# Optimization experiments

Measured on AMD Instinct MI355X. Metric: run time of the kernel, lower is better.

Reference implementation:

```python
import jax, jax.numpy as jnp
import numpy as np

B, T = 8192, 2048
DT = 1.0


def setup_inputs() -> dict:
    key = jax.random.key(0)
    k1, k2, k3 = jax.random.split(key, 3)
    price = jax.random.normal(k1, (B, T), dtype=jnp.float32)
    hurst = jax.random.uniform(k2, (B, T), dtype=jnp.float32)
    vol_sigma = jax.random.uniform(k3, (B, T), dtype=jnp.float32)
    return {"price": price, "hurst": hurst, "vol_sigma": vol_sigma}


def _ekf(price, hurst, vol_sigma):
    dt = DT
    b = price.shape[0]
    dtype = price.dtype
    eye2 = jnp.eye(2, dtype=dtype)
    # initial state: [price_0, (price_1 - price_0)/dt]
    v0 = (price[:, 1] - price[:, 0]) / dt
    x0 = jnp.stack([price[:, 0], v0], axis=1)               # [B,2]
    P0 = jnp.broadcast_to(eye2, (b, 2, 2))                  # [B,2,2]

    e1 = jnp.array([1.0, 0.0], dtype=dtype)                 # H row = [1,0]

    def step(carry, inp):
        x, P = carry                                        # [B,2], [B,2,2]
        z, h, sig = inp                                     # each [B]
        rho = 0.5 + 0.5 * jax.nn.sigmoid(10.0 * (h - 0.5))
        a = dt * rho                                        # F[:,0,1]
        ones = jnp.ones_like(a)
        zeros = jnp.zeros_like(a)
        # F = [[1, a],[0, 1]] per batch element
        F = jnp.stack([jnp.stack([ones, a], -1),
                       jnp.stack([zeros, ones], -1)], axis=1)  # [B,2,2]
        scale = jnp.maximum(100.0 * sig, 1.0)               # clamp(min=1)
        # predict
        x_pred = jnp.einsum('bij,bj->bi', F, x)
        P_pred = jnp.einsum('bij,bjk,blk->bil', F, P, F) \
                 + (0.1 * scale)[:, None, None] * eye2      # + Q
        # update (H = [1,0] observes position only)
        y = z - x_pred[:, 0]                                # residual [B]
        S = P_pred[:, 0, 0] + scale                         # + R
        S_inv = 1.0 / (S + 1e-6)
        K = P_pred[:, :, 0] * S_inv[:, None]                # [B,2]
        x_new = x_pred + K * y[:, None]
        ImKH = eye2 - K[:, :, None] * e1[None, None, :]     # I - K H
        P_new = jnp.einsum('bij,bjk->bik', ImKH, P_pred)
        return (x_new, P_new), x_new

    xs = (price.T, hurst.T, vol_sigma.T)                    # [T,B] each
    _, states = jax.lax.scan(step, (x0, P0), xs)            # states: [T,B,2]
    return jnp.transpose(states, (1, 0, 2))                 # [B,T,2]


def reference(price, hurst, vol_sigma):
    return _ekf(price, hurst, vol_sigma)
```

## Files before the change

kernel.cpp:

```cpp
#include <hip/hip_runtime.h>


#define NB 8192
#define NT 2048
#define TPB 128
#define SEG 16
#define NC4 4
#define LSTRIDE 130

__device__ __forceinline__ float frcp(float x)  { return __builtin_amdgcn_rcpf(x); }
__device__ __forceinline__ float fexp2(float x) { return __builtin_amdgcn_exp2f(x); }

struct Elt {
    float A00, A01, A10, A11;
    float b0, b1;
    float C00, C01, C11;
    float e0, e1;
    float J00, J01, J11;
};

__device__ __forceinline__ Elt combine(const Elt& i, const Elt& j)
{
    float D00 = 1.0f + __builtin_fmaf(i.C00, j.J00, i.C01 * j.J01);
    float D01 =        __builtin_fmaf(i.C00, j.J01, i.C01 * j.J11);
    float D10 =        __builtin_fmaf(i.C01, j.J00, i.C11 * j.J01);
    float D11 = 1.0f + __builtin_fmaf(i.C01, j.J01, i.C11 * j.J11);
    float idet = frcp(__builtin_fmaf(D00, D11, -D01 * D10));
    float V00 =  D11 * idet, V01 = -D01 * idet;
    float V10 = -D10 * idet, V11 =  D00 * idet;
    float E00 = __builtin_fmaf(j.A00, V00, j.A01 * V10);
    float E01 = __builtin_fmaf(j.A00, V01, j.A01 * V11);
    float E10 = __builtin_fmaf(j.A10, V00, j.A11 * V10);
    float E11 = __builtin_fmaf(j.A10, V01, j.A11 * V11);
    Elt r;
    r.A00 = __builtin_fmaf(E00, i.A00, E01 * i.A10);
    r.A01 = __builtin_fmaf(E00, i.A01, E01 * i.A11);
    r.A10 = __builtin_fmaf(E10, i.A00, E11 * i.A10);
    r.A11 = __builtin_fmaf(E10, i.A01, E11 * i.A11);
    float t0 = i.b0 + __builtin_fmaf(i.C00, j.e0, i.C01 * j.e1);
    float t1 = i.b1 + __builtin_fmaf(i.C01, j.e0, i.C11 * j.e1);
    r.b0 = j.b0 + __builtin_fmaf(E00, t0, E01 * t1);
    r.b1 = j.b1 + __builtin_fmaf(E10, t0, E11 * t1);
    float T00 = __builtin_fmaf(E00, i.C00, E01 * i.C01);
    float T01 = __builtin_fmaf(E00, i.C01, E01 * i.C11);
    float T10 = __builtin_fmaf(E10, i.C00, E11 * i.C01);
    float T11 = __builtin_fmaf(E10, i.C01, E11 * i.C11);
    r.C00 = j.C00 + __builtin_fmaf(T00, j.A00, T01 * j.A01);
    r.C01 = j.C01 + __builtin_fmaf(T00, j.A10, T01 * j.A11);
    r.C11 = j.C11 + __builtin_fmaf(T10, j.A10, T11 * j.A11);
    float u0 = j.e0 - __builtin_fmaf(j.J00, i.b0, j.J01 * i.b1);
    float u1 = j.e1 - __builtin_fmaf(j.J01, i.b0, j.J11 * i.b1);
    float w0 = __builtin_fmaf(V00, u0, V10 * u1);
    float w1 = __builtin_fmaf(V01, u0, V11 * u1);
    r.e0 = i.e0 + __builtin_fmaf(i.A00, w0, i.A10 * w1);
    r.e1 = i.e1 + __builtin_fmaf(i.A01, w0, i.A11 * w1);
    float W00 = __builtin_fmaf(V00, j.J00, V10 * j.J01);
    float W01 = __builtin_fmaf(V00, j.J01, V10 * j.J11);
    float W10 = __builtin_fmaf(V01, j.J00, V11 * j.J01);
    float W11 = __builtin_fmaf(V01, j.J01, V11 * j.J11);
    float X00 = __builtin_fmaf(i.A00, W00, i.A10 * W10);
    float X01 = __builtin_fmaf(i.A00, W01, i.A10 * W11);
    float X10 = __builtin_fmaf(i.A01, W00, i.A11 * W10);
    float X11 = __builtin_fmaf(i.A01, W01, i.A11 * W11);
    r.J00 = i.J00 + __builtin_fmaf(X00, i.A00, X01 * i.A10);
    r.J01 = i.J01 + __builtin_fmaf(X00, i.A01, X01 * i.A11);
    r.J11 = i.J11 + __builtin_fmaf(X10, i.A01, X11 * i.A11);
    return r;
}

__device__ __forceinline__ void append_step(Elt& E, float z, float h, float sg,
                                            float& a_out, float& sc_out)
{
    float ee = fexp2(__builtin_fmaf(h, -14.4269504088896f, 7.2134752044448f));
    float a  = __builtin_fmaf(0.5f, frcp(1.0f + ee), 0.5f);
    float sc = fmaxf(100.0f * sg, 1.0f);
    float q  = 0.1f * sc;
    float r  = sc + 1e-6f;
    float Sinv = frcp(q + r);
    float u = q * Sinv;
    float v = r * Sinv;
    a_out = a; sc_out = sc;

    float cw0 = __builtin_fmaf(a, E.C01, E.C00);
    float cw1 = __builtin_fmaf(a, E.C11, E.C01);
    float g0 = Sinv * cw0, g1 = Sinv * cw1;
    float rho = frcp(__builtin_fmaf(a, g1, 1.0f + g0));
    float gp0 = rho * g0, gp1 = rho * g1;

    float s0 = __builtin_fmaf(a, E.A10, E.A00);
    float s1 = __builtin_fmaf(a, E.A11, E.A01);

    float wb0  = __builtin_fmaf(a, E.b1, E.b0);
    float beta = Sinv * (z - wb0);
    float bp0  = __builtin_fmaf(z, g0, E.b0);
    float bp1  = __builtin_fmaf(z, g1, E.b1);

    float N00 = __builtin_fmaf(-gp0, s0, E.A00);
    float N01 = __builtin_fmaf(-gp0, s1, E.A01);
    float N10 = __builtin_fmaf(-gp1, s0, E.A10);
    float N11 = __builtin_fmaf(-gp1, s1, E.A11);
    float A00n = v * __builtin_fmaf(a, N10, N00);
    float A01n = v * __builtin_fmaf(a, N11, N01);
    float wbp = __builtin_fmaf(a, bp1, bp0);
    float t0b = __builtin_fmaf(-gp0, wbp, bp0);
    float t1b = __builtin_fmaf(-gp1, wbp, bp1);
    float b0n = __builtin_fmaf(v, __builtin_fmaf(a, t1b, t0b), u * z);
    float M00 = __builtin_fmaf(-gp0, cw0, E.C00);
    float M01 = __builtin_fmaf(-gp0, cw1, E.C01);
    float M11 = __builtin_fmaf(-gp1, cw1, E.C11);
    float tc0 = __builtin_fmaf(a, M01, M00);
    float tc1 = __builtin_fmaf(a, M11, M01);
    float C00n = v * __builtin_fmaf(v, __builtin_fmaf(a, tc1, tc0), q);
    float C01n = v * tc1;
    float C11n = M11 + q;
    float br  = beta * rho;
    float e0n = __builtin_fmaf(br, s0, E.e0);
    float e1n = __builtin_fmaf(br, s1, E.e1);
    float kap = rho * Sinv;
    float ks0 = kap * s0, ks1 = kap * s1;
    float J00n = __builtin_fmaf(ks0, s0, E.J00);
    float J01n = __builtin_fmaf(ks0, s1, E.J01);
    float J11n = __builtin_fmaf(ks1, s1, E.J11);

    E.A00 = A00n; E.A01 = A01n; E.A10 = N10; E.A11 = N11;
    E.b0 = b0n;  E.b1 = t1b;
    E.C00 = C00n; E.C01 = C01n; E.C11 = C11n;
    E.e0 = e0n;  E.e1 = e1n;
    E.J00 = J00n; E.J01 = J01n; E.J11 = J11n;
}

__device__ __forceinline__ Elt shfl_up_elt(const Elt& x, int d)
{
    Elt r;
    r.A00 = __shfl_up(x.A00, d, 64); r.A01 = __shfl_up(x.A01, d, 64);
    r.A10 = __shfl_up(x.A10, d, 64); r.A11 = __shfl_up(x.A11, d, 64);
    r.b0  = __shfl_up(x.b0,  d, 64); r.b1  = __shfl_up(x.b1,  d, 64);
    r.C00 = __shfl_up(x.C00, d, 64); r.C01 = __shfl_up(x.C01, d, 64);
    r.C11 = __shfl_up(x.C11, d, 64);
    r.e0  = __shfl_up(x.e0,  d, 64); r.e1  = __shfl_up(x.e1,  d, 64);
    r.J00 = __shfl_up(x.J00, d, 64); r.J01 = __shfl_up(x.J01, d, 64);
    r.J11 = __shfl_up(x.J11, d, 64);
    return r;
}

__device__ __forceinline__ void replay_step(float z, float a, float sc,
        float& x0, float& x1, float& p00, float& p01, float& p11)
{
    float q  = 0.1f * sc;
    float rp = sc + 1e-6f;
    float qr = q + rp;
    float tA = __builtin_fmaf(a + a, p01, p00);
    float tB = __builtin_fmaf(a * a, p11, qr);
    float Seff = tA + tB;
    float Sinv = frcp(Seff);
    float pp00 = Seff - rp;
    float pp01 = __builtin_fmaf(a, p11, p01);
    float pp11 = p11 + q;
    float K0 = pp00 * Sinv, K1 = pp01 * Sinv;
    float xp0 = __builtin_fmaf(a, x1, x0);
    float y = z - xp0;
    x0 = __builtin_fmaf(K0, y, xp0);
    x1 = __builtin_fmaf(K1, y, x1);
    p00 = __builtin_fmaf(-K0, pp00, pp00);
    p01 = __builtin_fmaf(-K0, pp01, pp01);
    p11 = __builtin_fmaf(-K1, pp01, pp11);
}

__global__ __launch_bounds__(TPB)
void ekf_kernel(const float* __restrict__ price,
                const float* __restrict__ hurst,
                const float* __restrict__ sigv,
                float* __restrict__ out)
{
    __shared__ float2 xlds[SEG][LSTRIDE];
    __shared__ float  w0tot[14];

    const int row  = blockIdx.x;
    const int tid  = threadIdx.x;
    const int lane = tid & 63;
    const int wav  = tid >> 6;

    const float4* __restrict__ pr4 = (const float4*)(price + (size_t)row * NT) + tid * NC4;
    const float4* __restrict__ hu4 = (const float4*)(hurst + (size_t)row * NT) + tid * NC4;
    const float4* __restrict__ sg4 = (const float4*)(sigv  + (size_t)row * NT) + tid * NC4;

    const float* __restrict__ prow = price + (size_t)row * NT;
    const float m00 = prow[0];
    const float m01 = prow[1] - m00;

    Elt E;
    E.A00 = 1.0f; E.A01 = 0.0f; E.A10 = 0.0f; E.A11 = 1.0f;
    E.b0 = 0.0f; E.b1 = 0.0f;
    E.C00 = 0.0f; E.C01 = 0.0f; E.C11 = 0.0f;
    E.e0 = 0.0f; E.e1 = 0.0f;
    E.J00 = 0.0f; E.J01 = 0.0f; E.J11 = 0.0f;
    {
        float4 zb[NC4], hb[NC4], sb[NC4];
#pragma unroll
        for (int c = 0; c < NC4; ++c) zb[c] = pr4[c];
#pragma unroll
        for (int c = 0; c < NC4; ++c) hb[c] = hu4[c];
#pragma unroll
        for (int c = 0; c < NC4; ++c) sb[c] = sg4[c];

#pragma unroll
        for (int c = 0; c < NC4; ++c) {
            float a0, c0, a1, c1, a2, c2, a3, c3;
            append_step(E, zb[c].x, hb[c].x, sb[c].x, a0, c0);
            append_step(E, zb[c].y, hb[c].y, sb[c].y, a1, c1);
            append_step(E, zb[c].z, hb[c].z, sb[c].z, a2, c2);
            append_step(E, zb[c].w, hb[c].w, sb[c].w, a3, c3);
            const int k = 4 * c;
            xlds[k + 0][tid] = make_float2(a0, c0);
            xlds[k + 1][tid] = make_float2(a1, c1);
            xlds[k + 2][tid] = make_float2(a2, c2);
            xlds[k + 3][tid] = make_float2(a3, c3);
        }
    }

#pragma unroll
    for (int d = 1; d < 64; d <<= 1) {
        Elt o = shfl_up_elt(E, d);
        Elt c = combine(o, E);
        bool p = (lane >= d);
        E.A00 = p ? c.A00 : E.A00; E.A01 = p ? c.A01 : E.A01;
        E.A10 = p ? c.A10 : E.A10; E.A11 = p ? c.A11 : E.A11;
        E.b0  = p ? c.b0  : E.b0;  E.b1  = p ? c.b1  : E.b1;
        E.C00 = p ? c.C00 : E.C00; E.C01 = p ? c.C01 : E.C01;
        E.C11 = p ? c.C11 : E.C11;
        E.e0  = p ? c.e0  : E.e0;  E.e1  = p ? c.e1  : E.e1;
        E.J00 = p ? c.J00 : E.J00; E.J01 = p ? c.J01 : E.J01;
        E.J11 = p ? c.J11 : E.J11;
    }

    if (tid == 63) {
        w0tot[0]  = E.A00; w0tot[1]  = E.A01; w0tot[2]  = E.A10; w0tot[3]  = E.A11;
        w0tot[4]  = E.b0;  w0tot[5]  = E.b1;
        w0tot[6]  = E.C00; w0tot[7]  = E.C01; w0tot[8]  = E.C11;
        w0tot[9]  = E.e0;  w0tot[10] = E.e1;
        w0tot[11] = E.J00; w0tot[12] = E.J01; w0tot[13] = E.J11;
    }
    __syncthreads();

    Elt ex = shfl_up_elt(E, 1);
    {
        bool l0 = (lane == 0);
        ex.A00 = l0 ? 1.0f : ex.A00; ex.A01 = l0 ? 0.0f : ex.A01;
        ex.A10 = l0 ? 0.0f : ex.A10; ex.A11 = l0 ? 1.0f : ex.A11;
        ex.b0  = l0 ? 0.0f : ex.b0;  ex.b1  = l0 ? 0.0f : ex.b1;
        ex.C00 = l0 ? 0.0f : ex.C00; ex.C01 = l0 ? 0.0f : ex.C01;
        ex.C11 = l0 ? 0.0f : ex.C11;
        ex.e0  = l0 ? 0.0f : ex.e0;  ex.e1  = l0 ? 0.0f : ex.e1;
        ex.J00 = l0 ? 0.0f : ex.J00; ex.J01 = l0 ? 0.0f : ex.J01;
        ex.J11 = l0 ? 0.0f : ex.J11;
    }
    if (wav == 1) {
        Elt w0;
        w0.A00 = w0tot[0];  w0.A01 = w0tot[1];  w0.A10 = w0tot[2];  w0.A11 = w0tot[3];
        w0.b0  = w0tot[4];  w0.b1  = w0tot[5];
        w0.C00 = w0tot[6];  w0.C01 = w0tot[7];  w0.C11 = w0tot[8];
        w0.e0  = w0tot[9];  w0.e1  = w0tot[10];
        w0.J00 = w0tot[11]; w0.J01 = w0tot[12]; w0.J11 = w0tot[13];
        ex = combine(w0, ex);
    }

    float D00 = 1.0f + ex.J00, D01 = ex.J01, D11 = 1.0f + ex.J11;
    float idet = frcp(__builtin_fmaf(D00, D11, -D01 * D01));
    float V00 =  D11 * idet, V01 = -D01 * idet;
    float V10 = -D01 * idet, V11 =  D00 * idet;
    float E00 = __builtin_fmaf(ex.A00, V00, ex.A01 * V10);
    float E01 = __builtin_fmaf(ex.A00, V01, ex.A01 * V11);
    float E10 = __builtin_fmaf(ex.A10, V00, ex.A11 * V10);
    float E11 = __builtin_fmaf(ex.A10, V01, ex.A11 * V11);
    float t0 = m00 + ex.e0, t1 = m01 + ex.e1;
    float x0 = ex.b0 + __builtin_fmaf(E00, t0, E01 * t1);
    float x1 = ex.b1 + __builtin_fmaf(E10, t0, E11 * t1);
    float p00 = ex.C00 + __builtin_fmaf(E00, ex.A00, E01 * ex.A01);
    float p01 = ex.C01 + __builtin_fmaf(E00, ex.A10, E01 * ex.A11);
    float p11 = ex.C11 + __builtin_fmaf(E10, ex.A10, E11 * ex.A11);

    {
        float4 zb[NC4];
#pragma unroll
        for (int c = 0; c < NC4; ++c) zb[c] = pr4[c];

#pragma unroll
        for (int c = 0; c < NC4; ++c) {
            const int k = 4 * c;
            float2 q0 = xlds[k + 0][tid];
            float2 q1 = xlds[k + 1][tid];
            float2 q2 = xlds[k + 2][tid];
            float2 q3 = xlds[k + 3][tid];

            replay_step(zb[c].x, q0.x, q0.y, x0, x1, p00, p01, p11);
            xlds[k + 0][tid] = make_float2(x0, x1);
            replay_step(zb[c].y, q1.x, q1.y, x0, x1, p00, p01, p11);
            xlds[k + 1][tid] = make_float2(x0, x1);
            replay_step(zb[c].z, q2.x, q2.y, x0, x1, p00, p01, p11);
            xlds[k + 2][tid] = make_float2(x0, x1);
            replay_step(zb[c].w, q3.x, q3.y, x0, x1, p00, p01, p11);
            xlds[k + 3][tid] = make_float2(x0, x1);
        }
    }
    __syncthreads();

    float2* __restrict__ op2 = (float2*)(out + (size_t)row * (size_t)NT * 2);
#pragma unroll
    for (int w = 0; w < SEG; ++w) {
        int n = w * TPB + tid;
        op2[n] = xlds[n & 15][n >> 4];
    }
}

extern "C" void kernel_launch(void* const* d_in, const int* in_sizes, int n_in,
                              void* d_out, int out_size, void* d_ws, size_t ws_size,
                              hipStream_t stream)
{
    const float* price = (const float*)d_in[0];
    const float* hurst = (const float*)d_in[1];
    const float* sigv  = (const float*)d_in[2];
    float* out = (float*)d_out;

    dim3 grid(NB), block(TPB);
    hipLaunchKernelGGL(ekf_kernel, grid, block, 0, stream, price, hurst, sigv, out);
}
```

Before: 278.0 us.

## Keep per-step coefficients in registers and write outputs directly from each thread

The per-step (a, scale) coefficients are now kept in a 16-entry register array instead of being staged in LDS. The LDS transpose buffer and its barrier are removed, and each thread stores its 16 contiguous float2 outputs straight to global memory. This cuts LDS traffic and a __syncthreads, but raises register pressure and makes the global stores strided across lanes (128 B apart) rather than fully coalesced.

Result: slower. 308.0 us (+10.8%).

```diff
diff --git a/kernel.cpp b/kernel.cpp
--- a/kernel.cpp
+++ b/kernel.cpp
@@ -6,7 +6,6 @@
 #define TPB 128
 #define SEG 16
 #define NC4 4
-#define LSTRIDE 130
 
 __device__ __forceinline__ float frcp(float x)  { return __builtin_amdgcn_rcpf(x); }
 __device__ __forceinline__ float fexp2(float x) { return __builtin_amdgcn_exp2f(x); }
@@ -68,18 +67,21 @@
     return r;
 }
 
-__device__ __forceinline__ void append_step(Elt& E, float z, float h, float sg,
-                                            float& a_out, float& sc_out)
+__device__ __forceinline__ float2 cvt_asc(float h, float sg)
 {
     float ee = fexp2(__builtin_fmaf(h, -14.4269504088896f, 7.2134752044448f));
     float a  = __builtin_fmaf(0.5f, frcp(1.0f + ee), 0.5f);
     float sc = fmaxf(100.0f * sg, 1.0f);
+    return make_float2(a, sc);
+}
+
+__device__ __forceinline__ void append_step(Elt& E, float z, float a, float sc)
+{
     float q  = 0.1f * sc;
     float r  = sc + 1e-6f;
     float Sinv = frcp(q + r);
     float u = q * Sinv;
     float v = r * Sinv;
-    a_out = a; sc_out = sc;
 
     float cw0 = __builtin_fmaf(a, E.C01, E.C00);
     float cw1 = __builtin_fmaf(a, E.C11, E.C01);
@@ -172,8 +174,7 @@
                 const float* __restrict__ sigv,
                 float* __restrict__ out)
 {
-    __shared__ float2 xlds[SEG][LSTRIDE];
-    __shared__ float  w0tot[14];
+    __shared__ float w0tot[14];
 
     const int row  = blockIdx.x;
     const int tid  = threadIdx.x;
@@ -188,6 +189,7 @@
     const float m00 = prow[0];
     const float m01 = prow[1] - m00;
 
+    float2 asc[SEG];
     Elt E;
     E.A00 = 1.0f; E.A01 = 0.0f; E.A10 = 0.0f; E.A11 = 1.0f;
     E.b0 = 0.0f; E.b1 = 0.0f;
@@ -205,16 +207,14 @@
 
 #pragma unroll
         for (int c = 0; c < NC4; ++c) {
-            float a0, c0, a1, c1, a2, c2, a3, c3;
-            append_step(E, zb[c].x, hb[c].x, sb[c].x, a0, c0);
-            append_step(E, zb[c].y, hb[c].y, sb[c].y, a1, c1);
-            append_step(E, zb[c].z, hb[c].z, sb[c].z, a2, c2);
-            append_step(E, zb[c].w, hb[c].w, sb[c].w, a3, c3);
-            const int k = 4 * c;
-            xlds[k + 0][tid] = make_float2(a0, c0);
-            xlds[k + 1][tid] = make_float2(a1, c1);
-            xlds[k + 2][tid] = make_float2(a2, c2);
-            xlds[k + 3][tid] = make_float2(a3, c3);
+            asc[4 * c + 0] = cvt_asc(hb[c].x, sb[c].x);
+            append_step(E, zb[c].x, asc[4 * c + 0].x, asc[4 * c + 0].y);
+            asc[4 * c + 1] = cvt_asc(hb[c].y, sb[c].y);
+            append_step(E, zb[c].y, asc[4 * c + 1].x, asc[4 * c + 1].y);
+            asc[4 * c + 2] = cvt_asc(hb[c].z, sb[c].z);
+            append_step(E, zb[c].z, asc[4 * c + 2].x, asc[4 * c + 2].y);
+            asc[4 * c + 3] = cvt_asc(hb[c].w, sb[c].w);
+            append_step(E, zb[c].w, asc[4 * c + 3].x, asc[4 * c + 3].y);
         }
     }
 
@@ -279,6 +279,7 @@
     float p01 = ex.C01 + __builtin_fmaf(E00, ex.A10, E01 * ex.A11);
     float p11 = ex.C11 + __builtin_fmaf(E10, ex.A10, E11 * ex.A11);
 
+    float2* __restrict__ op2 = (float2*)(out + (size_t)row * (size_t)NT * 2) + (size_t)tid * SEG;
     {
         float4 zb[NC4];
 #pragma unroll
@@ -286,29 +287,15 @@
 
 #pragma unroll
         for (int c = 0; c < NC4; ++c) {
-            const int k = 4 * c;
-            float2 q0 = xlds[k + 0][tid];
-            float2 q1 = xlds[k + 1][tid];
-            float2 q2 = xlds[k + 2][tid];
-            float2 q3 = xlds[k + 3][tid];
-
-            replay_step(zb[c].x, q0.x, q0.y, x0, x1, p00, p01, p11);
-            xlds[k + 0][tid] = make_float2(x0, x1);
-            replay_step(zb[c].y, q1.x, q1.y, x0, x1, p00, p01, p11);
-            xlds[k + 1][tid] = make_float2(x0, x1);
-            replay_step(zb[c].z, q2.x, q2.y, x0, x1, p00, p01, p11);
-            xlds[k + 2][tid] = make_float2(x0, x1);
-            replay_step(zb[c].w, q3.x, q3.y, x0, x1, p00, p01, p11);
-            xlds[k + 3][tid] = make_float2(x0, x1);
+            replay_step(zb[c].x, asc[4 * c + 0].x, asc[4 * c + 0].y, x0, x1, p00, p01, p11);
+            op2[4 * c + 0] = make_float2(x0, x1);
+            replay_step(zb[c].y, asc[4 * c + 1].x, asc[4 * c + 1].y, x0, x1, p00, p01, p11);
+            op2[4 * c + 1] = make_float2(x0, x1);
+            replay_step(zb[c].z, asc[4 * c + 2].x, asc[4 * c + 2].y, x0, x1, p00, p01, p11);
+            op2[4 * c + 2] = make_float2(x0, x1);
+            replay_step(zb[c].w, asc[4 * c + 3].x, asc[4 * c + 3].y, x0, x1, p00, p01, p11);
+            op2[4 * c + 3] = make_float2(x0, x1);
         }
-    }
-    __syncthreads();
-
-    float2* __restrict__ op2 = (float2*)(out + (size_t)row * (size_t)NT * 2);
-#pragma unroll
-    for (int w = 0; w < SEG; ++w) {
-        int n = w * TPB + tid;
-        op2[n] = xlds[n & 15][n >> 4];
     }
 }
 
```
